# Kernel tuning notes

Hardware: AMD Instinct MI355X
Metric: run time of the kernel (lower is better)

## Reference

```python
import jax, jax.numpy as jnp
import numpy as np

NHID, NHEAD, HEAD_DIM, U = 512, 16, 64, 3  # U = unfold_size (hardcoded 3 in original)
B, L = 8, 2048
D = NHEAD * HEAD_DIM  # 1024


def setup_inputs() -> dict:
    key = jax.random.key(0)
    ks = jax.random.split(key, 9)
    s = 0.02
    return {
        "x": jax.random.normal(ks[0], (B, NHID, L, 1), jnp.float32),
        "wq": jax.random.normal(ks[1], (NHID, D), jnp.float32) * s,
        "bq": jnp.zeros((D,), jnp.float32),
        "wk": jax.random.normal(ks[2], (NHID, D), jnp.float32) * s,
        "bk": jnp.zeros((D,), jnp.float32),
        "wv": jax.random.normal(ks[3], (NHID, D), jnp.float32) * s,
        "bv": jnp.zeros((D,), jnp.float32),
        "wo": jax.random.normal(ks[4], (D, NHID), jnp.float32) * s,
        "bo": jnp.zeros((NHID,), jnp.float32),
    }


def _unfold(t):
    # t: (B, D, L). Replicates tf.image.extract_patches (ksize 3, SAME, zero pad)
    # followed by the original's reshape (B,L,1,D,3) -- which reinterprets the
    # window-major flat layout (w*D + c) as (c', w') -- then transpose to
    # (B, D, 3, L) and reshape to (B, nhead, head_dim, 3, L).
    b, d, l = t.shape
    tt = jnp.transpose(t, (0, 2, 1))                  # (B, L, D)
    tp = jnp.pad(tt, ((0, 0), (1, 1), (0, 0)))        # SAME zero padding along L
    p = jnp.stack([tp[:, w:w + l, :] for w in range(U)], axis=2)  # (B, L, 3, D), flat idx = w*D + c
    p = p.reshape(b, l, d, U)                         # faithful reinterpreting reshape
    p = jnp.transpose(p, (0, 2, 3, 1))                # (B, D, 3, L)
    return p.reshape(b, NHEAD, HEAD_DIM, U, l)


def reference(x, wq, bq, wk, bk, wv, bv, wo, bo):
    b, c, l, _ = x.shape
    xs = x[..., 0]                                    # (B, C, L)
    # 1x1 convs (channels_first) == channel matmuls
    q = jnp.einsum('bcl,cd->bdl', xs, wq) + bq[None, :, None]
    k = jnp.einsum('bcl,cd->bdl', xs, wk) + bk[None, :, None]
    v = jnp.einsum('bcl,cd->bdl', xs, wv) + bv[None, :, None]
    q = q.reshape(b, NHEAD, HEAD_DIM, 1, l)           # (B, nh, hd, 1, L)
    k = _unfold(k)                                    # (B, nh, hd, 3, L)
    v = _unfold(v)
    scale = jnp.sqrt(jnp.asarray(HEAD_DIM, x.dtype))
    alphas = jnp.sum(q * k, axis=2, keepdims=True) / scale  # (B, nh, 1, 3, L)
    alphas = jax.nn.softmax(alphas, axis=3)
    att = jnp.sum(alphas * v, axis=3)                 # (B, nh, hd, L)
    # faithful to original: transpose then reinterpreting reshape to (B, D, L)
    att = jnp.transpose(att, (0, 1, 3, 2)).reshape(b, D, l)
    ret = jnp.einsum('bdl,dc->bcl', att, wo) + bo[None, :, None]
    return ret[..., None]                             # (B, nhid, L, 1)
```

## Files before the change

### kernel.cpp

```cpp
#include <hip/hip_runtime.h>

typedef _Float16 f16_t;
typedef _Float16 f16x2 __attribute__((ext_vector_type(2)));
typedef _Float16 f16x8 __attribute__((ext_vector_type(8)));
typedef float floatx4 __attribute__((ext_vector_type(4)));
typedef unsigned int u32;
typedef const __attribute__((address_space(1))) unsigned int* gptr_as1;
typedef __attribute__((address_space(3))) unsigned int* lptr_as3;

#define B_ 8
#define C_ 512
#define L_ 2048
#define D_ 1024
#define H_ 16

static __device__ __forceinline__ f16x2 bc2(u32 v) { return __builtin_bit_cast(f16x2, v); }
static __device__ __forceinline__ u32 cb2(f16x2 v) { return __builtin_bit_cast(u32, v); }

__global__ __launch_bounds__(256) void _MSA1_ktransf2h(const float* __restrict__ in,
                                                       f16_t* __restrict__ out,
                                                       int R, int C) {
  size_t zoff = (size_t)blockIdx.z * R * C;
  in += zoff; out += zoff;
  __shared__ f16_t tile[64][65];
  int r0 = blockIdx.y * 64, c0 = blockIdx.x * 64;
  int t = threadIdx.x;
  #pragma unroll
  for (int i = 0; i < 16; ++i) {
    int idx = t + i * 256;
    int r = idx >> 6, c = idx & 63;
    tile[c][r] = (f16_t)in[(size_t)(r0 + r) * C + (c0 + c)];
  }
  __syncthreads();
  #pragma unroll
  for (int i = 0; i < 16; ++i) {
    int idx = t + i * 256;
    int r = idx >> 6, c = idx & 63;
    out[(size_t)(c0 + r) * R + (r0 + c)] = tile[r][c];
  }
}

__global__ __launch_bounds__(256) void _MSA1_kprep(
    const float* __restrict__ wq, const float* __restrict__ wk,
    const float* __restrict__ wv, const float* __restrict__ wo,
    const float* __restrict__ bq, const float* __restrict__ bk,
    const float* __restrict__ bv,
    f16_t* __restrict__ wT3, f16_t* __restrict__ woT, float* __restrict__ bias3) {
  const int x = blockIdx.x, y = blockIdx.y;
  const int t = threadIdx.x;
  if (x == 128) {
    if (y == 0) {
      for (int i = t; i < 1024; i += 256) {
        bias3[i] = bq[i];
        bias3[1024 + i] = bk[i];
        bias3[2048 + i] = bv[i];
      }
    }
    return;
  }
  __shared__ f16_t tile[64][65];
  const float* in; f16_t* out; int R, C, r0, c0;
  if (y < 3) {
    R = 512; C = 1024;
    in = (y == 0) ? wq : (y == 1) ? wk : wv;
    out = wT3 + (size_t)y * 524288;
    r0 = (x >> 4) * 64; c0 = (x & 15) * 64;
  } else {
    R = 1024; C = 512;
    in = wo; out = woT;
    r0 = (x >> 3) * 64; c0 = (x & 7) * 64;
  }
  #pragma unroll
  for (int i = 0; i < 16; ++i) {
    int idx = t + i * 256;
    int r = idx >> 6, c = idx & 63;
    tile[c][r] = (f16_t)in[(size_t)(r0 + r) * C + (c0 + c)];
  }
  __syncthreads();
  #pragma unroll
  for (int i = 0; i < 16; ++i) {
    int idx = t + i * 256;
    int r = idx >> 6, c = idx & 63;
    out[(size_t)(c0 + r) * R + (r0 + c)] = tile[r][c];
  }
}

template <bool F32OUT, int K>
__global__ __launch_bounds__(256, 2) void _MSA1_kgemm(
    const f16_t* __restrict__ A, const f16_t* __restrict__ Bt,
    const float* __restrict__ bias, void* __restrict__ Cdv,
    int M, int N, long sA, long sB, long sC) {
  A  += (size_t)blockIdx.z * sA;
  Bt += (size_t)blockIdx.z * sB;
  const int m0 = blockIdx.y * 256, n0 = blockIdx.x * 128;

  union __align__(16) ShU {
    struct { f16_t As[3][256][32]; f16_t Bs[3][128][32]; } ab;
    f16_t Ep[F32OUT ? 1 : 64][132];
  };
  __shared__ ShU sh;

  const int t = threadIdx.x;
  const int lane = t & 63, w = t >> 6;
  const int mh = (w & 1) * 128, nh = (w >> 1) * 64;
  const int fm = lane & 15, fq = lane >> 4;
  const int srcswz = ((t & 3) ^ ((t >> 2) & 3) ^ ((t >> 4) & 3)) * 8;
  const int colf = ((fq ^ (fm & 3) ^ ((fm >> 2) & 3)) * 8);

  floatx4 acc[8][4];
  #pragma unroll
  for (int i = 0; i < 8; ++i)
    #pragma unroll
    for (int j = 0; j < 4; ++j) {
      floatx4 z4 = {0.f, 0.f, 0.f, 0.f};
      acc[i][j] = z4;
    }

  auto STAGE = [&](int kt, int bi) {
    #pragma unroll
    for (int j = 0; j < 4; ++j) {
      int r = (j * 256 + t) >> 2;
      const f16_t* ga = A + (size_t)(m0 + r) * K + kt + srcswz;
      __builtin_amdgcn_global_load_lds((gptr_as1)(const void*)ga,
          (lptr_as3)(void*)((char*)&sh.ab.As[bi][0][0] + j * 4096 + w * 1024), 16, 0, 0);
    }
    #pragma unroll
    for (int j = 0; j < 2; ++j) {
      int r = (j * 256 + t) >> 2;
      const f16_t* gb = Bt + (size_t)(n0 + r) * K + kt + srcswz;
      __builtin_amdgcn_global_load_lds((gptr_as1)(const void*)gb,
          (lptr_as3)(void*)((char*)&sh.ab.Bs[bi][0][0] + j * 4096 + w * 1024), 16, 0, 0);
    }
  };

  STAGE(0, 0);
  STAGE(32, 1);
  __builtin_amdgcn_sched_barrier(0);
  asm volatile("s_waitcnt vmcnt(6)" ::: "memory");
  __builtin_amdgcn_s_barrier();
  __builtin_amdgcn_sched_barrier(0);

  int bcur = 0;
  for (int kt = 0; kt < K; kt += 32) {
    if (kt + 64 < K) {
      int bi = bcur + 2; if (bi >= 3) bi -= 3;
      STAGE(kt + 64, bi);
    }
    f16x8 af[8], bfr[4];
    #pragma unroll
    for (int mt = 0; mt < 8; ++mt)
      af[mt] = *(const f16x8*)&sh.ab.As[bcur][mh + mt * 16 + fm][colf];
    #pragma unroll
    for (int nt = 0; nt < 4; ++nt)
      bfr[nt] = *(const f16x8*)&sh.ab.Bs[bcur][nh + nt * 16 + fm][colf];
    __builtin_amdgcn_s_setprio(1);
    #pragma unroll
    for (int mt = 0; mt < 8; ++mt)
      #pragma unroll
      for (int nt = 0; nt < 4; ++nt)
        acc[mt][nt] = __builtin_amdgcn_mfma_f32_16x16x32_f16(
            af[mt], bfr[nt], acc[mt][nt], 0, 0, 0);
    __builtin_amdgcn_s_setprio(0);
    if (kt + 32 < K) {
      __builtin_amdgcn_sched_barrier(0);
      if (kt + 64 < K)
        asm volatile("s_waitcnt vmcnt(6) lgkmcnt(0)" ::: "memory");
      else
        asm volatile("s_waitcnt vmcnt(0) lgkmcnt(0)" ::: "memory");
      __builtin_amdgcn_s_barrier();
      __builtin_amdgcn_sched_barrier(0);
    }
    bcur = (bcur == 2) ? 0 : bcur + 1;
  }
  __syncthreads();

  if (F32OUT) {
    float* Cd = (float*)Cdv + (size_t)blockIdx.z * sC;
    #pragma unroll
    for (int mt = 0; mt < 8; ++mt) {
      float bv4[4];
      #pragma unroll
      for (int r = 0; r < 4; ++r)
        bv4[r] = bias[m0 + mh + mt * 16 + fq * 4 + r];
      #pragma unroll
      for (int nt = 0; nt < 4; ++nt) {
        int col = n0 + nh + nt * 16 + fm;
        #pragma unroll
        for (int r = 0; r < 4; ++r) {
          int row = m0 + mh + mt * 16 + fq * 4 + r;
          Cd[(size_t)row * N + col] = acc[mt][nt][r] + bv4[r];
        }
      }
    }
  } else {
    f16_t* Cd = (f16_t*)Cdv + (size_t)blockIdx.z * sC;
    #pragma unroll
    for (int p = 0; p < 4; ++p) {
      if (p) __syncthreads();
      if ((w & 1) == (p >> 1)) {
        #pragma unroll
        for (int mt2 = 0; mt2 < 4; ++mt2) {
          int mt = (p & 1) * 4 + mt2;
          float bv4[4];
          #pragma unroll
          for (int r = 0; r < 4; ++r)
            bv4[r] = bias[m0 + p * 64 + mt2 * 16 + fq * 4 + r];
          #pragma unroll
          for (int nt = 0; nt < 4; ++nt) {
            int col = nh + nt * 16 + fm;
            #pragma unroll
            for (int r = 0; r < 4; ++r) {
              int row = mt2 * 16 + fq * 4 + r;
              sh.Ep[row][col] = (f16_t)(acc[mt][nt][r] + bv4[r]);
            }
          }
        }
      }
      __syncthreads();
      #pragma unroll
      for (int i = 0; i < 8; ++i) {
        int chunk = i * 256 + t;
        int row = chunk >> 5, c8 = chunk & 31;
        uint2 val = *(const uint2*)&sh.Ep[row][c8 * 4];
        *(uint2*)&Cd[(size_t)(m0 + p * 64 + row) * N + n0 + c8 * 4] = val;
      }
    }
  }
}

__global__ __launch_bounds__(256) void _MSA1_kattn6(const f16_t* __restrict__ qkv,
                                                    f16_t* __restrict__ attT) {
  const int t = threadIdx.x;
  const int lane = t & 63;
  const int wid = __builtin_amdgcn_readfirstlane(t >> 6);
  const int hb = blockIdx.x;
  const int h = hb & 15, b = hb >> 4;
  const int chi = blockIdx.y;
  const int lbase = chi * 256;
  const int l0 = lbase + lane * 4;
  const size_t plane = (size_t)D_ * L_;
  const f16_t* base = qkv + (size_t)b * 3 * plane;

  __shared__ uint2 sred[4][3][64];
  __shared__ __align__(16) f16_t tile2[2048][8];

  const f16_t* qp = base + (size_t)(h * 64 + wid * 16) * L_ + l0;
  const f16_t* kpl = base + plane;
  const f16_t* vpl = base + 2 * plane;
  const int g0 = h * 192 + wid * 48;

  f16x2 sLo[3], sHi[3];
  #pragma unroll
  for (int w = 0; w < 3; ++w) { f16x2 z = {(f16_t)0, (f16_t)0}; sLo[w] = z; sHi[w] = z; }

  #pragma unroll
  for (int dd = 0; dd < 16; ++dd) {
    uint2 qw = *(const uint2*)(qp + (size_t)dd * L_);
    f16x2 qlo = bc2(qw.x), qhi = bc2(qw.y);
    #pragma unroll
    for (int w = 0; w < 3; ++w) {
      int g = g0 + 3 * dd + w;
      int c = g & 1023;
      int o = (g >> 10) - 1;
      uint2 kw = *(const uint2*)(kpl + (size_t)c * L_ + (l0 + o));
      if (o < 0 && l0 == 0) kw.x &= 0xFFFF0000u;
      if (o > 0 && l0 == 2044) kw.y &= 0x0000FFFFu;
      sLo[w] = bc2(kw.x) * qlo + sLo[w];
      sHi[w] = bc2(kw.y) * qhi + sHi[w];
    }
  }
  #pragma unroll
  for (int w = 0; w < 3; ++w) {
    uint2 v; v.x = cb2(sLo[w]); v.y = cb2(sHi[w]);
    sred[wid][w][lane] = v;
  }
  __syncthreads();

  float sc[4][3];
  #pragma unroll
  for (int j = 0; j < 3; ++j) {
    uint2 r0 = sred[0][j][lane], r1 = sred[1][j][lane];
    uint2 r2 = sred[2][j][lane], r3 = sred[3][j][lane];
    f16x2 lo = (bc2(r0.x) + bc2(r1.x)) + (bc2(r2.x) + bc2(r3.x));
    f16x2 hi = (bc2(r0.y) + bc2(r1.y)) + (bc2(r2.y) + bc2(r3.y));
    sc[0][j] = (float)lo.x * 0.125f;
    sc[1][j] = (float)lo.y * 0.125f;
    sc[2][j] = (float)hi.x * 0.125f;
    sc[3][j] = (float)hi.y * 0.125f;
  }
  f16_t ef[4][3];
  #pragma unroll
  for (int li = 0; li < 4; ++li) {
    float mx = fmaxf(sc[li][0], fmaxf(sc[li][1], sc[li][2]));
    float e0 = __expf(sc[li][0] - mx), e1 = __expf(sc[li][1] - mx), e2 = __expf(sc[li][2] - mx);
    float inv = 1.f / (e0 + e1 + e2);
    ef[li][0] = (f16_t)(e0 * inv); ef[li][1] = (f16_t)(e1 * inv); ef[li][2] = (f16_t)(e2 * inv);
  }
  f16x2 eLo[3], eHi[3];
  #pragma unroll
  for (int w = 0; w < 3; ++w) {
    f16x2 a = {ef[0][w], ef[1][w]}; eLo[w] = a;
    f16x2 b2 = {ef[2][w], ef[3][w]}; eHi[w] = b2;
  }

  const int llb = (lane & 7) * 256 + wid * 16;
  const int jcol = lane >> 3;
  #pragma unroll
  for (int dd = 0; dd < 16; ++dd) {
    f16x2 aLo = {(f16_t)0, (f16_t)0}, aHi = {(f16_t)0, (f16_t)0};
    #pragma unroll
    for (int w = 0; w < 3; ++w) {
      int g = g0 + 3 * dd + w;
      int c = g & 1023;
      int o = (g >> 10) - 1;
      uint2 vw = *(const uint2*)(vpl + (size_t)c * L_ + (l0 + o));
      if (o < 0 && l0 == 0) vw.x &= 0xFFFF0000u;
      if (o > 0 && l0 == 2044) vw.y &= 0x0000FFFFu;
      aLo = bc2(vw.x) * eLo[w] + aLo;
      aHi = bc2(vw.y) * eHi[w] + aHi;
    }
    const int llq = llb + dd;
    tile2[llq +   0][jcol] = aLo.x;
    tile2[llq +  64][jcol] = aLo.y;
    tile2[llq + 128][jcol] = aHi.x;
    tile2[llq + 192][jcol] = aHi.y;
  }
  __syncthreads();

  f16_t* ob = attT + (size_t)b * L_ * D_ + h * 64 + chi * 8;
  #pragma unroll
  for (int i = 0; i < 8; ++i) {
    int ll = i * 256 + t;
    uint4 val = *(const uint4*)&tile2[ll][0];
    *(uint4*)(ob + (size_t)ll * D_) = val;
  }
}

extern "C" void kernel_launch(void* const* d_in, const int* in_sizes, int n_in,
                              void* d_out, int out_size, void* d_ws, size_t ws_size,
                              hipStream_t stream) {
  (void)in_sizes; (void)n_in; (void)out_size;
  const float* x  = (const float*)d_in[0];
  const float* wq = (const float*)d_in[1];
  const float* bq = (const float*)d_in[2];
  const float* wk = (const float*)d_in[3];
  const float* bk = (const float*)d_in[4];
  const float* wv = (const float*)d_in[5];
  const float* bv = (const float*)d_in[6];
  const float* wo = (const float*)d_in[7];
  const float* bo = (const float*)d_in[8];
  float* out = (float*)d_out;
  char* ws = (char*)d_ws;

  f16_t* wT3   = (f16_t*)(ws);
  f16_t* woT   = (f16_t*)(ws + 3145728);
  float* bias3 = (float*) (ws + 4194304);
  const size_t SHARED_END = 4210688;

  _MSA1_kprep<<<dim3(129, 4), dim3(256), 0, stream>>>(
      wq, wk, wv, wo, bq, bk, bv, wT3, woT, bias3);

  if (ws_size >= 155205632ull) {
    f16_t* xT    = (f16_t*)(ws + SHARED_END);
    f16_t* qkv   = xT + 8388608ull;
    f16_t* att2T = qkv + 50331648ull;

    _MSA1_ktransf2h<<<dim3(32, 8, B_), dim3(256), 0, stream>>>(x, xT, 512, 2048);
    _MSA1_kgemm<false, 512><<<dim3(16, 12, B_), dim3(256), 0, stream>>>(
        wT3, xT, bias3, qkv, 3072, 2048,
        0L, (long)(2048 * 512), (long)(3072 * 2048));
    _MSA1_kattn6<<<dim3(128, 8), dim3(256), 0, stream>>>(qkv, att2T);
    _MSA1_kgemm<true, 1024><<<dim3(16, 2, B_), dim3(256), 0, stream>>>(
        woT, att2T, bo, out, 512, 2048,
        0L, (long)(2048 * 1024), (long)(512 * 2048));
  } else {
    f16_t* xTb    = (f16_t*)(ws + SHARED_END);
    f16_t* qkvb   = xTb + 1048576ull;
    f16_t* att2Tb = qkvb + 6291456ull;
    for (int b = 0; b < B_; ++b) {
      const float* xb = x + (size_t)b * C_ * L_;
      _MSA1_ktransf2h<<<dim3(32, 8, 1), dim3(256), 0, stream>>>(xb, xTb, 512, 2048);
      _MSA1_kgemm<false, 512><<<dim3(16, 12, 1), dim3(256), 0, stream>>>(
          wT3, xTb, bias3, qkvb, 3072, 2048, 0L, 0L, 0L);
      _MSA1_kattn6<<<dim3(16, 8), dim3(256), 0, stream>>>(qkvb, att2Tb);
      _MSA1_kgemm<true, 1024><<<dim3(16, 2, 1), dim3(256), 0, stream>>>(
          woT, att2Tb, bo, out + (size_t)b * C_ * L_, 512, 2048, 0L, 0L, 0L);
    }
  }
}
```

Measured before the change: 263.7 us.

## Add 8-wave 256x256 QKV GEMM with interleaved LDS loads and MFMA phases

Replaces the QKV projection GEMM with a new 512-thread kernel computing 256x256 output tiles. It double-buffers 64-wide K slices split into 32-wide halves, and interleaves async global-to-LDS loads with four MFMA phases per K step, each separated by barriers. The larger tile is meant to raise operand reuse, and the finer-grained schedule is meant to hide load latency. In exchange it uses 128 KB of LDS per block and more barriers, and may lower occupancy or the number of blocks per CU.

```diff
diff --git a/kernel.cpp b/kernel.cpp
--- a/kernel.cpp
+++ b/kernel.cpp
@@ -16,6 +16,8 @@
 
 static __device__ __forceinline__ f16x2 bc2(u32 v) { return __builtin_bit_cast(f16x2, v); }
 static __device__ __forceinline__ u32 cb2(f16x2 v) { return __builtin_bit_cast(u32, v); }
+
+#define SCHEDB() __builtin_amdgcn_sched_barrier(0)
 
 __global__ __launch_bounds__(256) void _MSA1_ktransf2h(const float* __restrict__ in,
                                                        f16_t* __restrict__ out,
@@ -85,6 +87,162 @@
   }
 }
 
+template <int K>
+__global__ __launch_bounds__(512, 2) void _MSA1_kgemm8(
+    const f16_t* __restrict__ A, const f16_t* __restrict__ Bt,
+    const float* __restrict__ bias, f16_t* __restrict__ Cd0,
+    int M, int N, long sB, long sC) {
+  constexpr int KT = K / 64;
+  const f16_t* Bz = Bt + (size_t)blockIdx.z * sB;
+  const int m0 = blockIdx.y * 256, n0 = blockIdx.x * 256;
+
+  union __align__(16) ShU {
+    f16_t AB[8][8192];
+    f16_t Ep[64][264];
+  };
+  __shared__ ShU sh;
+
+  const int t = threadIdx.x;
+  const int lane = t & 63;
+  const int wid = t >> 6;
+  const int wm = wid & 1, wn = wid >> 1;
+  const int mh = wm * 128, nh = wn * 64;
+  const int fm = lane & 15, fq = lane >> 4;
+  const int srcswz = ((t & 3) ^ ((t >> 2) & 3) ^ ((t >> 4) & 3)) * 8;
+  const int colf = ((fq ^ (fm & 3) ^ ((fm >> 2) & 3)) * 8);
+
+  floatx4 acc[8][4];
+  #pragma unroll
+  for (int i = 0; i < 8; ++i)
+    #pragma unroll
+    for (int j = 0; j < 4; ++j) {
+      floatx4 z4 = {0.f, 0.f, 0.f, 0.f};
+      acc[i][j] = z4;
+    }
+
+  auto SG = [&](int T, int ab, int kk) {
+    const int d = T & 1;
+    const f16_t* src = ab ? Bz : A;
+    const int base0 = ab ? n0 : m0;
+    char* ldsb = (char*)&sh.AB[(d * 2 + ab) * 2 + kk][0];
+    #pragma unroll
+    for (int j = 0; j < 2; ++j) {
+      int idx = j * 512 + t;
+      int r = idx >> 2;
+      const f16_t* g = src + (size_t)(base0 + r) * K + T * 64 + kk * 32 + srcswz;
+      __builtin_amdgcn_global_load_lds((gptr_as1)(const void*)g,
+          (lptr_as3)(void*)(ldsb + idx * 16), 16, 0, 0);
+    }
+  };
+  auto LDA4 = [&](f16x8* af, int d, int kk, int mhalf) {
+    #pragma unroll
+    for (int m2 = 0; m2 < 4; ++m2)
+      af[m2] = *(const f16x8*)&sh.AB[(d * 2 + 0) * 2 + kk]
+                  [(mh + mhalf * 64 + m2 * 16 + fm) * 32 + colf];
+  };
+  auto LDB4 = [&](f16x8* bf, int d, int kk) {
+    #pragma unroll
+    for (int nt = 0; nt < 4; ++nt)
+      bf[nt] = *(const f16x8*)&sh.AB[(d * 2 + 1) * 2 + kk]
+                  [(nh + nt * 16 + fm) * 32 + colf];
+  };
+  auto MM = [&](const f16x8* af, const f16x8* bf, int mhalf) {
+    __builtin_amdgcn_s_setprio(1);
+    #pragma unroll
+    for (int m2 = 0; m2 < 4; ++m2)
+      #pragma unroll
+      for (int nt = 0; nt < 4; ++nt)
+        acc[mhalf * 4 + m2][nt] = __builtin_amdgcn_mfma_f32_16x16x32_f16(
+            af[m2], bf[nt], acc[mhalf * 4 + m2][nt], 0, 0, 0);
+    __builtin_amdgcn_s_setprio(0);
+  };
+
+  SG(0, 1, 0); SG(0, 0, 0); SG(0, 1, 1); SG(0, 0, 1);
+  SG(1, 1, 0); SG(1, 0, 0); SG(1, 1, 1);
+  SCHEDB();
+  asm volatile("s_waitcnt vmcnt(10)" ::: "memory");
+  __builtin_amdgcn_s_barrier();
+  SCHEDB();
+
+  f16x8 af[4], bfr[4];
+  #pragma unroll
+  for (int i = 0; i < KT; ++i) {
+    const int d = i & 1;
+    LDB4(bfr, d, 0);
+    LDA4(af, d, 0, 0);
+    SCHEDB();
+    __builtin_amdgcn_s_barrier();
+    asm volatile("s_waitcnt lgkmcnt(0)" ::: "memory");
+    SCHEDB();
+    if (i + 1 < KT) SG(i + 1, 0, 1);
+    MM(af, bfr, 0);
+    LDA4(af, d, 0, 1);
+    SCHEDB();
+    if (i == KT - 1) {
+      asm volatile("s_waitcnt vmcnt(0)" ::: "memory");
+    } else {
+      asm volatile("s_waitcnt vmcnt(8)" ::: "memory");
+    }
+    __builtin_amdgcn_s_barrier();
+    asm volatile("s_waitcnt lgkmcnt(0)" ::: "memory");
+    SCHEDB();
+    if (i + 2 < KT) SG(i + 2, 1, 0);
+    MM(af, bfr, 1);
+    LDB4(bfr, d, 1);
+    LDA4(af, d, 1, 0);
+    SCHEDB();
+    __builtin_amdgcn_s_barrier();
+    asm volatile("s_waitcnt lgkmcnt(0)" ::: "memory");
+    SCHEDB();
+    if (i + 2 < KT) SG(i + 2, 0, 0);
+    MM(af, bfr, 0);
+    LDA4(af, d, 1, 1);
+    SCHEDB();
+    if (i + 1 < KT) {
+      asm volatile("s_waitcnt vmcnt(8)" ::: "memory");
+    }
+    __builtin_amdgcn_s_barrier();
+    asm volatile("s_waitcnt lgkmcnt(0)" ::: "memory");
+    SCHEDB();
+    if (i + 2 < KT) SG(i + 2, 1, 1);
+    MM(af, bfr, 1);
+  }
+  __syncthreads();
+
+  f16_t* Cd = Cd0 + (size_t)blockIdx.z * sC;
+  #pragma unroll
+  for (int p = 0; p < 4; ++p) {
+    if (p) __syncthreads();
+    if (wm == (p >> 1)) {
+      #pragma unroll
+      for (int m2 = 0; m2 < 4; ++m2) {
+        int mt = (p & 1) * 4 + m2;
+        float bv4[4];
+        #pragma unroll
+        for (int r = 0; r < 4; ++r)
+          bv4[r] = bias[m0 + p * 64 + m2 * 16 + fq * 4 + r];
+        #pragma unroll
+        for (int nt = 0; nt < 4; ++nt) {
+          int col = nh + nt * 16 + fm;
+          #pragma unroll
+          for (int r = 0; r < 4; ++r) {
+            int row = m2 * 16 + fq * 4 + r;
+            sh.Ep[row][col] = (f16_t)(acc[mt][nt][r] + bv4[r]);
+          }
+        }
+      }
+    }
+    __syncthreads();
+    #pragma unroll
+    for (int ii = 0; ii < 8; ++ii) {
+      int chunk = ii * 512 + t;
+      int row = chunk >> 6, c8 = chunk & 63;
+      uint2 val = *(const uint2*)&sh.Ep[row][c8 * 4];
+      *(uint2*)&Cd[(size_t)(m0 + p * 64 + row) * N + n0 + c8 * 4] = val;
+    }
+  }
+}
+
 template <bool F32OUT, int K>
 __global__ __launch_bounds__(256, 2) void _MSA1_kgemm(
     const f16_t* __restrict__ A, const f16_t* __restrict__ Bt,
@@ -135,10 +293,10 @@
 
   STAGE(0, 0);
   STAGE(32, 1);
-  __builtin_amdgcn_sched_barrier(0);
+  SCHEDB();
   asm volatile("s_waitcnt vmcnt(6)" ::: "memory");
   __builtin_amdgcn_s_barrier();
-  __builtin_amdgcn_sched_barrier(0);
+  SCHEDB();
 
   int bcur = 0;
   for (int kt = 0; kt < K; kt += 32) {
@@ -162,13 +320,13 @@
             af[mt], bfr[nt], acc[mt][nt], 0, 0, 0);
     __builtin_amdgcn_s_setprio(0);
     if (kt + 32 < K) {
-      __builtin_amdgcn_sched_barrier(0);
+      SCHEDB();
       if (kt + 64 < K)
         asm volatile("s_waitcnt vmcnt(6) lgkmcnt(0)" ::: "memory");
       else
         asm volatile("s_waitcnt vmcnt(0) lgkmcnt(0)" ::: "memory");
       __builtin_amdgcn_s_barrier();
-      __builtin_amdgcn_sched_barrier(0);
+      SCHEDB();
     }
     bcur = (bcur == 2) ? 0 : bcur + 1;
   }
@@ -366,9 +524,9 @@
     f16_t* att2T = qkv + 50331648ull;
 
     _MSA1_ktransf2h<<<dim3(32, 8, B_), dim3(256), 0, stream>>>(x, xT, 512, 2048);
-    _MSA1_kgemm<false, 512><<<dim3(16, 12, B_), dim3(256), 0, stream>>>(
+    _MSA1_kgemm8<512><<<dim3(8, 12, B_), dim3(512), 0, stream>>>(
         wT3, xT, bias3, qkv, 3072, 2048,
-        0L, (long)(2048 * 512), (long)(3072 * 2048));
+        (long)(2048 * 512), (long)(3072 * 2048));
     _MSA1_kattn6<<<dim3(128, 8), dim3(256), 0, stream>>>(qkv, att2T);
     _MSA1_kgemm<true, 1024><<<dim3(16, 2, B_), dim3(256), 0, stream>>>(
         woT, att2T, bo, out, 512, 2048,
@@ -380,8 +538,8 @@
     for (int b = 0; b < B_; ++b) {
       const float* xb = x + (size_t)b * C_ * L_;
       _MSA1_ktransf2h<<<dim3(32, 8, 1), dim3(256), 0, stream>>>(xb, xTb, 512, 2048);
-      _MSA1_kgemm<false, 512><<<dim3(16, 12, 1), dim3(256), 0, stream>>>(
-          wT3, xTb, bias3, qkvb, 3072, 2048, 0L, 0L, 0L);
+      _MSA1_kgemm8<512><<<dim3(8, 12, 1), dim3(512), 0, stream>>>(
+          wT3, xTb, bias3, qkvb, 3072, 2048, 0L, 0L);
       _MSA1_kattn6<<<dim3(16, 8), dim3(256), 0, stream>>>(qkvb, att2Tb);
       _MSA1_kgemm<true, 1024><<<dim3(16, 2, 1), dim3(256), 0, stream>>>(
           woT, att2Tb, bo, out + (size_t)b * C_ * L_, 512, 2048, 0L, 0L, 0L);
```

New measurement: 264.9 us. No clear change (+0.5%).
